# Performance work log

Measured on AMD Instinct MI355X. Metric: run time of the kernel, lower is better.

The kernel has to match this reference:

```python
import jax, jax.numpy as jnp
import numpy as np

NODE_NUM = 6
C_IN = 1024
B = 16384
N_OPS = 9
TAU = 10.0
EPS = 1e-5
ACTS = (jax.nn.relu, jax.nn.sigmoid, jnp.tanh)


def setup_inputs() -> dict:
    key = jax.random.key(0)
    k = jax.random.split(key, 12)
    n_edges = NODE_NUM * (NODE_NUM + 1) // 2  # 21
    nB = n_edges - NODE_NUM  # 15 edges with cin=cout=C_IN//2

    def w(kk, shape, fan_in):
        return jax.random.normal(kk, shape, jnp.float32) / np.float32(np.sqrt(fan_in))

    return {
        "x": jax.random.normal(k[0], (B, C_IN), jnp.float32),
        "arch_params": 0.001 * jax.random.normal(k[1], (n_edges, N_OPS), jnp.float32),
        "gumbel": jax.random.gumbel(k[2], (n_edges, N_OPS), jnp.float32),
        "dense_w_A": w(k[3], (NODE_NUM, 3, C_IN // 2, C_IN), C_IN),
        "dense_b_A": 0.01 * jax.random.normal(k[4], (NODE_NUM, 3, C_IN // 2), jnp.float32),
        "group_w_A": w(k[5], (NODE_NUM, 3, 4, C_IN // 8, C_IN // 4), C_IN // 4),
        "group_b_A": 0.01 * jax.random.normal(k[6], (NODE_NUM, 3, C_IN // 2), jnp.float32),
        "pool_w_A": w(k[7], (NODE_NUM, 2, C_IN // 2, C_IN), C_IN),
        "dense_w_B": w(k[8], (nB, 3, C_IN // 2, C_IN // 2), C_IN // 2),
        "dense_b_B": 0.01 * jax.random.normal(k[9], (nB, 3, C_IN // 2), jnp.float32),
        "group_w_B": w(k[10], (nB, 3, 4, C_IN // 8, C_IN // 8), C_IN // 8),
        "group_b_B": 0.01 * jax.random.normal(k[11], (nB, 3, C_IN // 2), jnp.float32),
    }


def _batchnorm(h):
    # training-mode BatchNorm2d on [B, C, 1, 1] == normalize over batch, affine-free
    m = jnp.mean(h, axis=0, keepdims=True)
    v = jnp.var(h, axis=0, keepdims=True)
    return (h - m) * jax.lax.rsqrt(v + EPS)


def _apply_edge(h, op_idx, wscale, dw, db, gw, gb, pw):
    # h: [B, cin]; dw: [3, cout, cin]; gw: [3, 4, cout//4, cin//4]; pw: [2, cout, cin] or None
    cout = dw.shape[1]

    def pool(p):
        def f(hh):
            # ReLU-Conv1x1-BN preprocess when cin != cout, else identity
            y = _batchnorm(jax.nn.relu(hh) @ pw[p].T) if pw is not None else hh
            if p == 0:  # avg_pool_3x3 on 1x1 spatial, pad=1, count_include_pad
                y = y / 9.0
            # p == 1: max_pool_3x3 on 1x1 spatial is identity
            return _batchnorm(y)  # MixedOp-appended BatchNorm2d(affine=False)
        return f

    def dense(a):
        return lambda hh: ACTS[a](hh @ dw[a].T + db[a])

    def gdense(a):
        def f(hh):
            hg = hh.reshape(hh.shape[0], 4, -1)  # [B, 4, cin//4]
            y = jnp.einsum('bgi,goi->bgo', hg, gw[a]).reshape(hh.shape[0], -1) + gb[a]
            return ACTS[a](y)
        return f

    zero = lambda hh: jnp.zeros((hh.shape[0], cout), hh.dtype)
    branches = [pool(0), pool(1), dense(0), dense(1), dense(2),
                gdense(0), gdense(1), gdense(2), zero]
    return jax.lax.switch(op_idx, branches, h) * wscale


def reference(x, arch_params, gumbel, dense_w_A, dense_b_A, group_w_A, group_b_A,
              pool_w_A, dense_w_B, dense_b_B, group_w_B, group_b_B):
    # GDAS gumbel-softmax hard routing (straight-through)
    logits = (jax.nn.log_softmax(arch_params, axis=1) + gumbel) / TAU
    prob = jax.nn.softmax(logits, axis=1)
    index = jnp.argmax(prob, axis=1)                      # [n_edges]
    one_h = jax.nn.one_hot(index, N_OPS, dtype=prob.dtype)
    hardwts = one_h - jax.lax.stop_gradient(prob) + prob  # [n_edges, N_OPS]

    # arch rows are indexed by sorted edge-key order, matching torch edge2index
    keys = sorted('{}->{}'.format(j, i + 1) for i in range(NODE_NUM) for j in range(i + 1))
    e2i = {kk: n for n, kk in enumerate(keys)}

    states = [x]
    a_ct = 0
    b_ct = 0
    for i in range(1, NODE_NUM + 1):
        acc = None
        for j in range(i):
            e = e2i['{}->{}'.format(j, i)]
            w_e = hardwts[e, index[e]]
            if j == 0:
                out = _apply_edge(states[0], index[e], w_e, dense_w_A[a_ct], dense_b_A[a_ct],
                                  group_w_A[a_ct], group_b_A[a_ct], pool_w_A[a_ct])
                a_ct += 1
            else:
                out = _apply_edge(states[j], index[e], w_e, dense_w_B[b_ct], dense_b_B[b_ct],
                                  group_w_B[b_ct], group_b_B[b_ct], None)
                b_ct += 1
            acc = out if acc is None else acc + out
        states.append(acc)
    return states[-1]  # [B, C_IN//2]; final_linear is never applied in forward()
```

## Files before the change

kernel.cpp:

```cpp
#include <hip/hip_runtime.h>

#define BATCH 16384
#define CH 512
#define EPSBN 1e-5f

typedef __attribute__((ext_vector_type(8))) short short8;
typedef __attribute__((ext_vector_type(4))) float f32x4;
typedef __attribute__((ext_vector_type(4))) unsigned short ushort4v;

#define GLOAD16(gp, lp) __builtin_amdgcn_global_load_lds( \
    (const __attribute__((address_space(1))) void*)(gp),  \
    (__attribute__((address_space(3))) void*)(lp), 16, 0, 0)

__constant__ int d_etab[6][6] = {
  {0,0,0,0,0,0},
  {1,6,0,0,0,0},
  {2,7,11,0,0,0},
  {3,8,12,15,0,0},
  {4,9,13,16,18,0},
  {5,10,14,17,19,20}};
__constant__ int d_bct[21] = {0,0,0,0,0,0, 0,1,3,6,10, 2,4,7,11, 5,8,12, 9,13, 14};

static __device__ __forceinline__ long woff(int e){
  return (e < 6) ? (long)e*524288 : 3145728L + (long)d_bct[e]*262144;
}

static __device__ __forceinline__ unsigned short f2b(float f){
  union { float f; unsigned u; } v; v.f = f;
  unsigned r = v.u + 0x7fffu + ((v.u >> 16) & 1u);
  return (unsigned short)(r >> 16);
}
static __device__ __forceinline__ float b2f(unsigned short u){
  union { unsigned u; float f; } v; v.u = ((unsigned)u) << 16; return v.f;
}
static __device__ __forceinline__ float actf(int act, float v){
  if (act == 0) return fmaxf(v, 0.f);
  if (act == 1) return 1.f/(1.f + __expf(-v));
  float e = __expf(2.f*v);
  return 1.f - 2.f/(e + 1.f);
}

__global__ void k_sentinel(float* out){ out[0] = 1.0e6f; }

__global__ void k_index(const float* __restrict__ ap, const float* __restrict__ gum,
                        int* __restrict__ idx, float* __restrict__ wsc){
  int e = threadIdx.x;
  if (e >= 21) return;
  const float* a = ap + e*9;
  const float* g = gum + e*9;
  float m = a[0];
  for (int o=1;o<9;o++) m = fmaxf(m, a[o]);
  float s = 0.f;
  for (int o=0;o<9;o++) s += expf(a[o]-m);
  float lse = m + logf(s);
  float lg[9]; float lm = -1e30f;
  for (int o=0;o<9;o++){ lg[o] = (a[o]-lse+g[o]) / 10.0f; lm = fmaxf(lm, lg[o]); }
  float ss = 0.f;
  for (int o=0;o<9;o++) ss += expf(lg[o]-lm);
  int bi = 0; float bp = -1.f;
  for (int o=0;o<9;o++){
    float p = expf(lg[o]-lm)/ss;
    if (p > bp){ bp = p; bi = o; }
  }
  idx[e] = bi;
  wsc[e] = (1.0f - bp) + bp;
}

__global__ void k_f2b4(const float* __restrict__ in, unsigned short* __restrict__ outp, long n4){
  long stride = (long)gridDim.x*blockDim.x;
  for (long i = (long)blockIdx.x*blockDim.x + threadIdx.x; i < n4; i += stride){
    const float4 v = ((const float4*)in)[i];
    ushort4v o;
    o[0] = f2b(v.x); o[1] = f2b(v.y); o[2] = f2b(v.z); o[3] = f2b(v.w);
    ((ushort4v*)outp)[i] = o;
  }
}

__global__ void k_wconv_all(const int* __restrict__ idxp,
                            const float* __restrict__ dwA, const float* __restrict__ pwA,
                            const float* __restrict__ gwA, const float* __restrict__ dwB,
                            const float* __restrict__ gwB,
                            unsigned short* __restrict__ Wball){
  int e = blockIdx.x >> 7;
  int blk = blockIdx.x & 127;
  int id = idxp[e];
  const float* src; long n;
  if (e < 6){
    int a = e;
    if (id >= 2 && id <= 4){ n = 524288; src = dwA + ((long)a*3 + (id-2))*n; }
    else if (id < 2)       { n = 524288; src = pwA + ((long)a*2 + id)*n; }
    else if (id <= 7)      { n = 131072; src = gwA + ((long)a*3 + (id-5))*131072; }
    else return;
  } else {
    int b = d_bct[e];
    if (id >= 2 && id <= 4)     { n = 262144; src = dwB + ((long)b*3 + (id-2))*n; }
    else if (id >= 5 && id <= 7){ n = 65536;  src = gwB + ((long)b*3 + (id-5))*65536; }
    else return;
  }
  unsigned short* dst = Wball + woff(e);
  long n4 = n >> 2;
  long stride = 128*256;
  for (long i = (long)blk*256 + threadIdx.x; i < n4; i += stride){
    const float4 v = ((const float4*)src)[i];
    ushort4v o;
    o[0] = f2b(v.x); o[1] = f2b(v.y); o[2] = f2b(v.z); o[3] = f2b(v.w);
    ((ushort4v*)dst)[i] = o;
  }
}

__global__ __launch_bounds__(512, 4) void k_gemm_pool(
    int node, const unsigned short* __restrict__ xb,
    const unsigned short* __restrict__ Wball, unsigned short* __restrict__ tmp,
    const int* __restrict__ idxp)
{
  int e = node - 1;
  int id = idxp[e];
  if (id >= 2) return;

  int bid = blockIdx.x;
  int lg = (bid & 7) * 64 + (bid >> 3);
  int rowTile = lg >> 2, colTile = lg & 3;
  int row0 = rowTile * 128, col0 = colTile * 128;

  int t = threadIdx.x;
  int lane = t & 63, wave = t >> 6;
  int wm = wave >> 2, wn = wave & 3;
  int l16 = lane & 15, lq = lane >> 4;

  __shared__ unsigned short LDS[24576];

  int ra = t >> 2;
  int ca = (((t & 3) ^ ((ra >> 1) & 3)) << 3);
  int aoff[4], boff[2];
  #pragma unroll
  for (int m=0;m<4;m++){ int R = wm*64 + m*16 + l16; aoff[m] = R*32 + ((lq ^ ((R>>1)&3))<<3); }
  #pragma unroll
  for (int n=0;n<2;n++){ int C = wn*32 + n*16 + l16; boff[n] = C*32 + ((lq ^ ((C>>1)&3))<<3); }

  const unsigned short* W = Wball + (long)e*524288 + (long)col0*1024;
  const unsigned short* gA = xb + (long)(row0 + ra)*1024 + ca;
  const unsigned short* gB = W  + (long)ra*1024 + ca;

  f32x4 acc[4][2];
  #pragma unroll
  for (int m=0;m<4;m++){ acc[m][0]=(f32x4){0,0,0,0}; acc[m][1]=(f32x4){0,0,0,0}; }

  auto STAGE = [&](int tile, int bsel){
    long kk = (long)tile*32;
    GLOAD16(gA + kk, &LDS[bsel*4096 + t*8]);
    GLOAD16(gB + kk, &LDS[12288 + bsel*4096 + t*8]);
  };

  const int nk = 32;
  STAGE(0, 0);
  STAGE(1, 1);
  int cb = 0;
  for (int kt = 0; kt < nk; ++kt){
    if (kt+1 < nk) { asm volatile("s_waitcnt vmcnt(2)" ::: "memory"); }
    else           { asm volatile("s_waitcnt vmcnt(0)" ::: "memory"); }
    __builtin_amdgcn_s_barrier();
    if (kt+2 < nk) STAGE(kt+2, (cb >= 1) ? cb-1 : cb+2);
    const unsigned short* pA = &LDS[cb*4096];
    const unsigned short* pB = &LDS[12288 + cb*4096];
    short8 a[4], b[2];
    #pragma unroll
    for (int m=0;m<4;m++){
      a[m] = *(const short8*)(pA + aoff[m]);
      #pragma unroll
      for (int q=0;q<8;q++) a[m][q] = (a[m][q] < (short)0) ? (short)0 : a[m][q];
    }
    #pragma unroll
    for (int n=0;n<2;n++) b[n] = *(const short8*)(pB + boff[n]);
    #pragma unroll
    for (int m=0;m<4;m++)
      #pragma unroll
      for (int n=0;n<2;n++)
        acc[m][n] = __builtin_amdgcn_mfma_f32_16x16x32_bf16(a[m], b[n], acc[m][n], 0,0,0);
    cb = (cb+1 == 3) ? 0 : cb+1;
  }

  #pragma unroll
  for (int n=0;n<2;n++){
    int cn = col0 + wn*32 + n*16 + l16;
    #pragma unroll
    for (int m=0;m<4;m++)
      #pragma unroll
      for (int r=0;r<4;r++){
        int row = row0 + wm*64 + m*16 + lq*4 + r;
        tmp[(long)row*CH + cn] = f2b(acc[m][n][r]);
      }
  }
}

__global__ __launch_bounds__(512) void k_stats_node(
    int node, const unsigned short* __restrict__ tmp,
    const unsigned short* __restrict__ sb0, const unsigned short* __restrict__ sb1,
    const unsigned short* __restrict__ sb2, const unsigned short* __restrict__ sb3,
    const unsigned short* __restrict__ sb4,
    float* __restrict__ part, const int* __restrict__ idxp)
{
  int c = threadIdx.x;
  for (int jj = 0; jj < node; ++jj){
    int e = d_etab[node-1][jj];
    if (idxp[e] >= 2) continue;
    const unsigned short* S;
    switch(jj){ case 0: S=tmp; break; case 1: S=sb0; break; case 2: S=sb1; break;
                case 3: S=sb2; break; case 4: S=sb3; break; default: S=sb4; }
    const unsigned short* p = S + (long)blockIdx.x*128*CH + c;
    float s = 0.f, q = 0.f;
    for (int r = 0; r < 128; r++){ float v = b2f(p[(long)r*CH]); s += v; q += v*v; }
    long o = (((long)jj*128 + blockIdx.x)*CH + c)*2;
    part[o] = s; part[o+1] = q;
  }
}

__global__ __launch_bounds__(512) void k_stats2_node(
    int node, const float* __restrict__ part,
    float* __restrict__ alphaAll, float* __restrict__ mvalAll,
    const int* __restrict__ idxp)
{
  int c = threadIdx.x;
  for (int jj = 0; jj < node; ++jj){
    int e = d_etab[node-1][jj];
    int id = idxp[e];
    if (id >= 2) continue;
    float s = 0.f, q = 0.f;
    for (int b = 0; b < 128; b++){
      long o = (((long)jj*128 + b)*CH + c)*2;
      s += part[o]; q += part[o+1];
    }
    float m = s * (1.f/16384.f);
    float v = q * (1.f/16384.f) - m*m;
    v = fmaxf(v, 0.f);
    float al;
    if (jj == 0){
      float s1 = rsqrtf(v + EPSBN);
      float vz = v / (v + EPSBN);
      al = (id==0) ? (s1 * (1.f/9.f) * rsqrtf(vz*(1.f/81.f) + EPSBN))
                   : (s1 * rsqrtf(vz + EPSBN));
    } else {
      al = (id==0) ? ((1.f/9.f) * rsqrtf(v*(1.f/81.f) + EPSBN))
                   : rsqrtf(v + EPSBN);
    }
    alphaAll[(long)e*CH + c] = al;
    mvalAll[(long)e*CH + c] = m;
  }
}

__global__ __launch_bounds__(512, 4) void k_fused(
    int node,
    const unsigned short* __restrict__ xb,
    const unsigned short* __restrict__ sb0, const unsigned short* __restrict__ sb1,
    const unsigned short* __restrict__ sb2, const unsigned short* __restrict__ sb3,
    const unsigned short* __restrict__ sb4,
    unsigned short* __restrict__ sbout, float* __restrict__ outf,
    const unsigned short* __restrict__ tmp, const unsigned short* __restrict__ Wball,
    const float* __restrict__ dbA, const float* __restrict__ gbA,
    const float* __restrict__ dbB, const float* __restrict__ gbB,
    const float* __restrict__ alphaAll, const float* __restrict__ mvalAll,
    const int* __restrict__ idxp, const float* __restrict__ wscp)
{
  int bid = blockIdx.x;
  int lg = (bid & 7) * 64 + (bid >> 3);
  int rowTile = lg >> 2, colTile = lg & 3;
  int row0 = rowTile * 128, col0 = colTile * 128;

  int t = threadIdx.x;
  int lane = t & 63, wave = t >> 6;
  int wm = wave >> 2, wn = wave & 3;
  int l16 = lane & 15, lq = lane >> 4;

  __shared__ unsigned short LDS[24576];

  int ra = t >> 2;
  int ca = (((t & 3) ^ ((ra >> 1) & 3)) << 3);
  int aoff[4], boff[2];
  #pragma unroll
  for (int m=0;m<4;m++){ int R = wm*64 + m*16 + l16; aoff[m] = R*32 + ((lq ^ ((R>>1)&3))<<3); }
  #pragma unroll
  for (int n=0;n<2;n++){ int C = wn*32 + n*16 + l16; boff[n] = C*32 + ((lq ^ ((C>>1)&3))<<3); }

  f32x4 facc[4][2];
  #pragma unroll
  for (int m=0;m<4;m++){ facc[m][0]=(f32x4){0,0,0,0}; facc[m][1]=(f32x4){0,0,0,0}; }

  for (int jj = 0; jj < node; ++jj){
    int e = d_etab[node-1][jj];
    int id = idxp[e];
    if (id == 8) continue;
    float we = wscp[e];

    const unsigned short* st;
    switch(jj){ case 0: st=xb; break; case 1: st=sb0; break; case 2: st=sb1; break;
                case 3: st=sb2; break; case 4: st=sb3; break; default: st=sb4; }

    if (id < 2){
      const unsigned short* S = (jj==0) ? tmp : st;
      const float* al = alphaAll + (long)e*CH;
      const float* mv = mvalAll + (long)e*CH;
      #pragma unroll
      for (int n=0;n<2;n++){
        int cn = col0 + wn*32 + n*16 + l16;
        float a_n = al[cn], m_n = mv[cn];
        #pragma unroll
        for (int m=0;m<4;m++){
          int rowb = row0 + wm*64 + m*16 + lq*4;
          #pragma unroll
          for (int r=0;r<4;r++)
            facc[m][n][r] += we * (b2f(S[(long)(rowb+r)*CH + cn]) - m_n) * a_n;
        }
      }
      continue;
    }

    bool grp = (id >= 5);
    int cin = (jj==0) ? 1024 : 512;
    int K = grp ? (cin >> 2) : cin;
    int act = grp ? id - 5 : id - 2;
    const unsigned short* Abase = st + (grp ? (long)colTile*K : 0);
    const unsigned short* Wbase = Wball + woff(e) + (long)col0*K;
    const float* bias;
    if (jj == 0) bias = (grp ? gbA : dbA) + ((long)e*3 + act)*CH;
    else         bias = (grp ? gbB : dbB) + ((long)d_bct[e]*3 + act)*CH;

    const unsigned short* gA = Abase + (long)(row0 + ra)*cin + ca;
    const unsigned short* gB = Wbase + (long)ra*K + ca;

    f32x4 acc[4][2];
    #pragma unroll
    for (int m=0;m<4;m++){ acc[m][0]=(f32x4){0,0,0,0}; acc[m][1]=(f32x4){0,0,0,0}; }

    auto STAGE = [&](int tile, int bsel){
      long kk = (long)tile*32;
      GLOAD16(gA + kk, &LDS[bsel*4096 + t*8]);
      GLOAD16(gB + kk, &LDS[12288 + bsel*4096 + t*8]);
    };

    int nk = K >> 5;
    __builtin_amdgcn_s_barrier();
    STAGE(0, 0);
    STAGE(1, 1);
    int cb = 0;
    for (int kt = 0; kt < nk; ++kt){
      if (kt+1 < nk) { asm volatile("s_waitcnt vmcnt(2)" ::: "memory"); }
      else           { asm volatile("s_waitcnt vmcnt(0)" ::: "memory"); }
      __builtin_amdgcn_s_barrier();
      if (kt+2 < nk) STAGE(kt+2, (cb >= 1) ? cb-1 : cb+2);
      const unsigned short* pA = &LDS[cb*4096];
      const unsigned short* pB = &LDS[12288 + cb*4096];
      short8 a[4], b[2];
      #pragma unroll
      for (int m=0;m<4;m++) a[m] = *(const short8*)(pA + aoff[m]);
      #pragma unroll
      for (int n=0;n<2;n++) b[n] = *(const short8*)(pB + boff[n]);
      #pragma unroll
      for (int m=0;m<4;m++)
        #pragma unroll
        for (int n=0;n<2;n++)
          acc[m][n] = __builtin_amdgcn_mfma_f32_16x16x32_bf16(a[m], b[n], acc[m][n], 0,0,0);
      cb = (cb+1 == 3) ? 0 : cb+1;
    }

    #pragma unroll
    for (int n=0;n<2;n++){
      int cn = col0 + wn*32 + n*16 + l16;
      float bv = bias[cn];
      #pragma unroll
      for (int m=0;m<4;m++)
        #pragma unroll
        for (int r=0;r<4;r++)
          facc[m][n][r] += we * actf(act, acc[m][n][r] + bv);
    }
  }

  #pragma unroll
  for (int n=0;n<2;n++){
    int cn = col0 + wn*32 + n*16 + l16;
    #pragma unroll
    for (int m=0;m<4;m++){
      int rowb = row0 + wm*64 + m*16 + lq*4;
      #pragma unroll
      for (int r=0;r<4;r++){
        long off = (long)(rowb+r)*CH + cn;
        if (node == 6) outf[off] = facc[m][n][r];
        else           sbout[off] = f2b(facc[m][n][r]);
      }
    }
  }
}

extern "C" void kernel_launch(void* const* d_in, const int* in_sizes, int n_in,
                              void* d_out, int out_size, void* d_ws, size_t ws_size,
                              hipStream_t stream)
{
  const float* x   = (const float*)d_in[0];
  const float* ap  = (const float*)d_in[1];
  const float* gum = (const float*)d_in[2];
  const float* dwA = (const float*)d_in[3];
  const float* dbA = (const float*)d_in[4];
  const float* gwA = (const float*)d_in[5];
  const float* gbA = (const float*)d_in[6];
  const float* pwA = (const float*)d_in[7];
  const float* dwB = (const float*)d_in[8];
  const float* dbB = (const float*)d_in[9];
  const float* gwB = (const float*)d_in[10];
  const float* gbB = (const float*)d_in[11];
  float* out = (float*)d_out;

  char* ws = (char*)d_ws;
  size_t cur = 0;
  auto alloc = [&](size_t bytes)->void*{
    size_t o = cur; cur += (bytes + 255) & ~(size_t)255; return (void*)(ws + o);
  };
  int*   idx      = (int*)  alloc(21*sizeof(int));
  float* wsc      = (float*)alloc(21*sizeof(float));
  float* alphaAll = (float*)alloc((size_t)21*CH*sizeof(float));
  float* mvalAll  = (float*)alloc((size_t)21*CH*sizeof(float));
  float* part     = (float*)alloc((size_t)6*128*CH*2*sizeof(float));
  unsigned short* Wball = (unsigned short*)alloc((size_t)7077888*sizeof(unsigned short));
  unsigned short* tmp   = (unsigned short*)alloc((size_t)BATCH*CH*sizeof(unsigned short));
  unsigned short* xb    = (unsigned short*)alloc((size_t)BATCH*1024*sizeof(unsigned short));
  unsigned short* sb[5];
  for (int i=0;i<5;i++)
    sb[i] = (unsigned short*)alloc((size_t)BATCH*CH*sizeof(unsigned short));

  if (cur > ws_size){
    hipLaunchKernelGGL(k_sentinel, dim3(1), dim3(1), 0, stream, out);
    return;
  }

  hipLaunchKernelGGL(k_f2b4, dim3(2048), dim3(256), 0, stream, x, xb, (long)BATCH*1024/4);
  hipLaunchKernelGGL(k_index, dim3(1), dim3(32), 0, stream, ap, gum, idx, wsc);
  hipLaunchKernelGGL(k_wconv_all, dim3(21*128), dim3(256), 0, stream,
                     idx, dwA, pwA, gwA, dwB, gwB, Wball);

  for (int node = 1; node <= 6; node++){
    hipLaunchKernelGGL(k_gemm_pool, dim3(512), dim3(512), 0, stream,
                       node, xb, Wball, tmp, idx);
    hipLaunchKernelGGL(k_stats_node, dim3(128), dim3(512), 0, stream,
                       node, tmp, sb[0], sb[1], sb[2], sb[3], sb[4], part, idx);
    hipLaunchKernelGGL(k_stats2_node, dim3(1), dim3(512), 0, stream,
                       node, part, alphaAll, mvalAll, idx);
    hipLaunchKernelGGL(k_fused, dim3(512), dim3(512), 0, stream,
                       node, xb, sb[0], sb[1], sb[2], sb[3], sb[4],
                       (node < 6) ? sb[node-1] : sb[0], out,
                       tmp, Wball, dbA, gbA, dbB, gbB,
                       alphaAll, mvalAll, idx, wsc);
  }
}
```

Measured before the change: 420.0 us.

## Load GEMM weight fragments directly to registers, stage only activations in LDS

In both the pool-preprocess GEMM and the fused node GEMM, the weight (B) operand is now read straight from global memory into registers, double-buffered across two k-steps. Only the activation (A) tile still goes through LDS via global_load_lds, which halves shared memory per block and removes the B-side LDS reads. The loop is unrolled by two and uses sched_barriers and vmcnt waits to overlap the register loads with MFMA work. The tradeoffs are uncoalesced 16-byte per-lane weight loads, more register pressure, and tighter vmcnt accounting that assumes a specific ordering of outstanding loads.

```diff
diff --git a/kernel.cpp b/kernel.cpp
--- a/kernel.cpp
+++ b/kernel.cpp
@@ -127,56 +127,69 @@
   int wm = wave >> 2, wn = wave & 3;
   int l16 = lane & 15, lq = lane >> 4;
 
-  __shared__ unsigned short LDS[24576];
+  __shared__ unsigned short LDS[12288];
 
   int ra = t >> 2;
   int ca = (((t & 3) ^ ((ra >> 1) & 3)) << 3);
-  int aoff[4], boff[2];
+  int aoff[4];
   #pragma unroll
   for (int m=0;m<4;m++){ int R = wm*64 + m*16 + l16; aoff[m] = R*32 + ((lq ^ ((R>>1)&3))<<3); }
-  #pragma unroll
-  for (int n=0;n<2;n++){ int C = wn*32 + n*16 + l16; boff[n] = C*32 + ((lq ^ ((C>>1)&3))<<3); }
-
-  const unsigned short* W = Wball + (long)e*524288 + (long)col0*1024;
-  const unsigned short* gA = xb + (long)(row0 + ra)*1024 + ca;
-  const unsigned short* gB = W  + (long)ra*1024 + ca;
+
+  const int K = 1024;
+  const unsigned short* Wbase = Wball + (long)e*524288 + (long)col0*K;
+  const unsigned short* bp0 = Wbase + (long)(wn*32 +  0 + l16)*K + lq*8;
+  const unsigned short* bp1 = Wbase + (long)(wn*32 + 16 + l16)*K + lq*8;
+  const unsigned short* gA = xb + (long)(row0 + ra)*K + ca;
 
   f32x4 acc[4][2];
   #pragma unroll
   for (int m=0;m<4;m++){ acc[m][0]=(f32x4){0,0,0,0}; acc[m][1]=(f32x4){0,0,0,0}; }
 
-  auto STAGE = [&](int tile, int bsel){
-    long kk = (long)tile*32;
-    GLOAD16(gA + kk, &LDS[bsel*4096 + t*8]);
-    GLOAD16(gB + kk, &LDS[12288 + bsel*4096 + t*8]);
+  auto COMPUTE = [&](const unsigned short* pA, const short8* b){
+    short8 a[4];
+    #pragma unroll
+    for (int m=0;m<4;m++){
+      a[m] = *(const short8*)(pA + aoff[m]);
+      #pragma unroll
+      for (int q=0;q<8;q++) a[m][q] = (a[m][q] < (short)0) ? (short)0 : a[m][q];
+    }
+    #pragma unroll
+    for (int m=0;m<4;m++)
+      #pragma unroll
+      for (int n=0;n<2;n++)
+        acc[m][n] = __builtin_amdgcn_mfma_f32_16x16x32_bf16(a[m], b[n], acc[m][n], 0,0,0);
   };
 
   const int nk = 32;
-  STAGE(0, 0);
-  STAGE(1, 1);
-  int cb = 0;
-  for (int kt = 0; kt < nk; ++kt){
-    if (kt+1 < nk) { asm volatile("s_waitcnt vmcnt(2)" ::: "memory"); }
+  short8 br0[2], br1[2];
+  br0[0] = *(const short8*)(bp0);
+  br0[1] = *(const short8*)(bp1);
+  __builtin_amdgcn_sched_barrier(0);
+  GLOAD16(gA,          &LDS[t*8]);
+  GLOAD16(gA + 32,     &LDS[4096 + t*8]);
+
+  int c0 = 0;
+  for (int kt = 0; kt < nk; kt += 2){
+    int c1 = c0+1; if (c1==3) c1=0;
+    int c2 = c1+1; if (c2==3) c2=0;
+    asm volatile("s_waitcnt vmcnt(1)" ::: "memory");
+    __builtin_amdgcn_s_barrier();
+    br1[0] = *(const short8*)(bp0 + (kt+1)*32);
+    br1[1] = *(const short8*)(bp1 + (kt+1)*32);
+    __builtin_amdgcn_sched_barrier(0);
+    if (kt+2 < nk) GLOAD16(gA + (long)(kt+2)*32, &LDS[c2*4096 + t*8]);
+    COMPUTE(&LDS[c0*4096], br0);
+    if (kt+2 < nk) { asm volatile("s_waitcnt vmcnt(1)" ::: "memory"); }
     else           { asm volatile("s_waitcnt vmcnt(0)" ::: "memory"); }
     __builtin_amdgcn_s_barrier();
-    if (kt+2 < nk) STAGE(kt+2, (cb >= 1) ? cb-1 : cb+2);
-    const unsigned short* pA = &LDS[cb*4096];
-    const unsigned short* pB = &LDS[12288 + cb*4096];
-    short8 a[4], b[2];
-    #pragma unroll
-    for (int m=0;m<4;m++){
-      a[m] = *(const short8*)(pA + aoff[m]);
-      #pragma unroll
-      for (int q=0;q<8;q++) a[m][q] = (a[m][q] < (short)0) ? (short)0 : a[m][q];
-    }
-    #pragma unroll
-    for (int n=0;n<2;n++) b[n] = *(const short8*)(pB + boff[n]);
-    #pragma unroll
-    for (int m=0;m<4;m++)
-      #pragma unroll
-      for (int n=0;n<2;n++)
-        acc[m][n] = __builtin_amdgcn_mfma_f32_16x16x32_bf16(a[m], b[n], acc[m][n], 0,0,0);
-    cb = (cb+1 == 3) ? 0 : cb+1;
+    if (kt+2 < nk){
+      br0[0] = *(const short8*)(bp0 + (kt+2)*32);
+      br0[1] = *(const short8*)(bp1 + (kt+2)*32);
+    }
+    __builtin_amdgcn_sched_barrier(0);
+    if (kt+3 < nk) GLOAD16(gA + (long)(kt+3)*32, &LDS[c0*4096 + t*8]);
+    COMPUTE(&LDS[c1*4096], br1);
+    c0 = c2;
   }
 
   #pragma unroll
@@ -270,15 +283,13 @@
   int wm = wave >> 2, wn = wave & 3;
   int l16 = lane & 15, lq = lane >> 4;
 
-  __shared__ unsigned short LDS[24576];
+  __shared__ unsigned short LDS[12288];
 
   int ra = t >> 2;
   int ca = (((t & 3) ^ ((ra >> 1) & 3)) << 3);
-  int aoff[4], boff[2];
+  int aoff[4];
   #pragma unroll
   for (int m=0;m<4;m++){ int R = wm*64 + m*16 + l16; aoff[m] = R*32 + ((lq ^ ((R>>1)&3))<<3); }
-  #pragma unroll
-  for (int n=0;n<2;n++){ int C = wn*32 + n*16 + l16; boff[n] = C*32 + ((lq ^ ((C>>1)&3))<<3); }
 
   f32x4 facc[4][2];
   #pragma unroll
@@ -323,42 +334,56 @@
     if (jj == 0) bias = (grp ? gbA : dbA) + ((long)e*3 + act)*CH;
     else         bias = (grp ? gbB : dbB) + ((long)d_bct[e]*3 + act)*CH;
 
+    const unsigned short* bp0 = Wbase + (long)(wn*32 +  0 + l16)*K + lq*8;
+    const unsigned short* bp1 = Wbase + (long)(wn*32 + 16 + l16)*K + lq*8;
     const unsigned short* gA = Abase + (long)(row0 + ra)*cin + ca;
-    const unsigned short* gB = Wbase + (long)ra*K + ca;
 
     f32x4 acc[4][2];
     #pragma unroll
     for (int m=0;m<4;m++){ acc[m][0]=(f32x4){0,0,0,0}; acc[m][1]=(f32x4){0,0,0,0}; }
 
-    auto STAGE = [&](int tile, int bsel){
-      long kk = (long)tile*32;
-      GLOAD16(gA + kk, &LDS[bsel*4096 + t*8]);
-      GLOAD16(gB + kk, &LDS[12288 + bsel*4096 + t*8]);
-    };
-
-    int nk = K >> 5;
-    __builtin_amdgcn_s_barrier();
-    STAGE(0, 0);
-    STAGE(1, 1);
-    int cb = 0;
-    for (int kt = 0; kt < nk; ++kt){
-      if (kt+1 < nk) { asm volatile("s_waitcnt vmcnt(2)" ::: "memory"); }
-      else           { asm volatile("s_waitcnt vmcnt(0)" ::: "memory"); }
-      __builtin_amdgcn_s_barrier();
-      if (kt+2 < nk) STAGE(kt+2, (cb >= 1) ? cb-1 : cb+2);
-      const unsigned short* pA = &LDS[cb*4096];
-      const unsigned short* pB = &LDS[12288 + cb*4096];
-      short8 a[4], b[2];
+    auto COMPUTE = [&](const unsigned short* pA, const short8* b){
+      short8 a[4];
       #pragma unroll
       for (int m=0;m<4;m++) a[m] = *(const short8*)(pA + aoff[m]);
-      #pragma unroll
-      for (int n=0;n<2;n++) b[n] = *(const short8*)(pB + boff[n]);
       #pragma unroll
       for (int m=0;m<4;m++)
         #pragma unroll
         for (int n=0;n<2;n++)
           acc[m][n] = __builtin_amdgcn_mfma_f32_16x16x32_bf16(a[m], b[n], acc[m][n], 0,0,0);
-      cb = (cb+1 == 3) ? 0 : cb+1;
+    };
+
+    int nk = K >> 5;
+    __builtin_amdgcn_s_barrier();
+    short8 br0[2], br1[2];
+    br0[0] = *(const short8*)(bp0);
+    br0[1] = *(const short8*)(bp1);
+    __builtin_amdgcn_sched_barrier(0);
+    GLOAD16(gA,      &LDS[t*8]);
+    GLOAD16(gA + 32, &LDS[4096 + t*8]);
+
+    int c0 = 0;
+    for (int kt = 0; kt < nk; kt += 2){
+      int c1 = c0+1; if (c1==3) c1=0;
+      int c2 = c1+1; if (c2==3) c2=0;
+      asm volatile("s_waitcnt vmcnt(1)" ::: "memory");
+      __builtin_amdgcn_s_barrier();
+      br1[0] = *(const short8*)(bp0 + (kt+1)*32);
+      br1[1] = *(const short8*)(bp1 + (kt+1)*32);
+      __builtin_amdgcn_sched_barrier(0);
+      if (kt+2 < nk) GLOAD16(gA + (long)(kt+2)*32, &LDS[c2*4096 + t*8]);
+      COMPUTE(&LDS[c0*4096], br0);
+      if (kt+2 < nk) { asm volatile("s_waitcnt vmcnt(1)" ::: "memory"); }
+      else           { asm volatile("s_waitcnt vmcnt(0)" ::: "memory"); }
+      __builtin_amdgcn_s_barrier();
+      if (kt+2 < nk){
+        br0[0] = *(const short8*)(bp0 + (kt+2)*32);
+        br0[1] = *(const short8*)(bp1 + (kt+2)*32);
+      }
+      __builtin_amdgcn_sched_barrier(0);
+      if (kt+3 < nk) GLOAD16(gA + (long)(kt+3)*32, &LDS[c0*4096 + t*8]);
+      COMPUTE(&LDS[c1*4096], br1);
+      c0 = c2;
     }
 
     #pragma unroll
```

Result: slower. 561.5 us (+33.7%).

## Batch all six x-input edge GEMMs into one launch before the node loop

Applied to the files above, without the earlier changes.

All six edges that read the input x (j=0) do not depend on earlier nodes, so one kernel now computes their GEMMs (pool, dense or grouped) together, writing pre-activation or activated results into per-node buffers. Their BN statistics are also gathered in one batched stats pass. The per-node fused kernel then only adds those precomputed outputs instead of redoing the K=1024 GEMM inside the sequential chain. This fills the GPU with a larger grid and removes per-node launches. In exchange it needs extra intermediate buffers and reuses the sb buffers in place, which makes the aliasing (pre and sbout pointing to the same buffer) subtle.

```diff
diff --git a/kernel.cpp b/kernel.cpp
--- a/kernel.cpp
+++ b/kernel.cpp
@@ -108,17 +108,28 @@
   }
 }
 
-__global__ __launch_bounds__(512, 4) void k_gemm_pool(
-    int node, const unsigned short* __restrict__ xb,
-    const unsigned short* __restrict__ Wball, unsigned short* __restrict__ tmp,
-    const int* __restrict__ idxp)
-{
-  int e = node - 1;
+__global__ __launch_bounds__(512, 4) void k_gemmA_all(
+    const unsigned short* __restrict__ xb, const unsigned short* __restrict__ Wball,
+    unsigned short* __restrict__ s0, unsigned short* __restrict__ s1,
+    unsigned short* __restrict__ s2, unsigned short* __restrict__ s3,
+    unsigned short* __restrict__ s4, unsigned short* __restrict__ pre6,
+    const float* __restrict__ dbA, const float* __restrict__ gbA,
+    const int* __restrict__ idxp, const float* __restrict__ wscp)
+{
+  int e = blockIdx.x >> 9;
   int id = idxp[e];
-  if (id >= 2) return;
-
-  int bid = blockIdx.x;
-  int lg = (bid & 7) * 64 + (bid >> 3);
+  if (id == 8) return;
+  unsigned short* target;
+  switch(e){ case 0: target=s0; break; case 1: target=s1; break; case 2: target=s2; break;
+             case 3: target=s3; break; case 4: target=s4; break; default: target=pre6; }
+  bool pool = (id < 2);
+  bool grp = (id >= 5);
+  int K = grp ? 256 : 1024;
+  int act = pool ? 0 : (grp ? id-5 : id-2);
+  float we = wscp[e];
+
+  int inner = blockIdx.x & 511;
+  int lg = (inner & 7) * 64 + (inner >> 3);
   int rowTile = lg >> 2, colTile = lg & 3;
   int row0 = rowTile * 128, col0 = colTile * 128;
 
@@ -137,9 +148,11 @@
   #pragma unroll
   for (int n=0;n<2;n++){ int C = wn*32 + n*16 + l16; boff[n] = C*32 + ((lq ^ ((C>>1)&3))<<3); }
 
-  const unsigned short* W = Wball + (long)e*524288 + (long)col0*1024;
-  const unsigned short* gA = xb + (long)(row0 + ra)*1024 + ca;
-  const unsigned short* gB = W  + (long)ra*1024 + ca;
+  const unsigned short* Abase = xb + (grp ? (long)colTile*K : 0);
+  const unsigned short* Wbase = Wball + (long)e*524288 + (long)col0*K;
+  const unsigned short* gA = Abase + (long)(row0 + ra)*1024 + ca;
+  const unsigned short* gB = Wbase + (long)ra*K + ca;
+  const float* bias = (grp ? gbA : dbA) + ((long)e*3 + act)*CH;
 
   f32x4 acc[4][2];
   #pragma unroll
@@ -151,7 +164,7 @@
     GLOAD16(gB + kk, &LDS[12288 + bsel*4096 + t*8]);
   };
 
-  const int nk = 32;
+  int nk = K >> 5;
   STAGE(0, 0);
   STAGE(1, 1);
   int cb = 0;
@@ -166,8 +179,10 @@
     #pragma unroll
     for (int m=0;m<4;m++){
       a[m] = *(const short8*)(pA + aoff[m]);
-      #pragma unroll
-      for (int q=0;q<8;q++) a[m][q] = (a[m][q] < (short)0) ? (short)0 : a[m][q];
+      if (pool){
+        #pragma unroll
+        for (int q=0;q<8;q++) a[m][q] = (a[m][q] < (short)0) ? (short)0 : a[m][q];
+      }
     }
     #pragma unroll
     for (int n=0;n<2;n++) b[n] = *(const short8*)(pB + boff[n]);
@@ -182,29 +197,77 @@
   #pragma unroll
   for (int n=0;n<2;n++){
     int cn = col0 + wn*32 + n*16 + l16;
+    float bv = pool ? 0.f : bias[cn];
     #pragma unroll
     for (int m=0;m<4;m++)
       #pragma unroll
       for (int r=0;r<4;r++){
         int row = row0 + wm*64 + m*16 + lq*4 + r;
-        tmp[(long)row*CH + cn] = f2b(acc[m][n][r]);
+        long off = (long)row*CH + cn;
+        if (pool) target[off] = f2b(acc[m][n][r]);
+        else      target[off] = f2b(we * actf(act, acc[m][n][r] + bv));
       }
   }
 }
 
-__global__ __launch_bounds__(512) void k_stats_node(
-    int node, const unsigned short* __restrict__ tmp,
+__global__ __launch_bounds__(512) void k_statsA(
+    const unsigned short* __restrict__ s0, const unsigned short* __restrict__ s1,
+    const unsigned short* __restrict__ s2, const unsigned short* __restrict__ s3,
+    const unsigned short* __restrict__ s4, const unsigned short* __restrict__ pre6,
+    float* __restrict__ part, const int* __restrict__ idxp)
+{
+  int e = blockIdx.x >> 7;
+  if (idxp[e] >= 2) return;
+  const unsigned short* S;
+  switch(e){ case 0: S=s0; break; case 1: S=s1; break; case 2: S=s2; break;
+             case 3: S=s3; break; case 4: S=s4; break; default: S=pre6; }
+  int blk = blockIdx.x & 127;
+  int c = threadIdx.x;
+  const unsigned short* p = S + (long)blk*128*CH + c;
+  float s = 0.f, q = 0.f;
+  for (int r = 0; r < 128; r++){ float v = b2f(p[(long)r*CH]); s += v; q += v*v; }
+  long o = (((long)e*128 + blk)*CH + c)*2;
+  part[o] = s; part[o+1] = q;
+}
+
+__global__ __launch_bounds__(512) void k_stats2A(
+    const float* __restrict__ part, float* __restrict__ alphaAll,
+    float* __restrict__ mvalAll, const int* __restrict__ idxp)
+{
+  int c = threadIdx.x;
+  for (int e = 0; e < 6; ++e){
+    int id = idxp[e];
+    if (id >= 2) continue;
+    float s = 0.f, q = 0.f;
+    for (int b = 0; b < 128; b++){
+      long o = (((long)e*128 + b)*CH + c)*2;
+      s += part[o]; q += part[o+1];
+    }
+    float m = s * (1.f/16384.f);
+    float v = q * (1.f/16384.f) - m*m;
+    v = fmaxf(v, 0.f);
+    float s1 = rsqrtf(v + EPSBN);
+    float vz = v / (v + EPSBN);
+    float al = (id==0) ? (s1 * (1.f/9.f) * rsqrtf(vz*(1.f/81.f) + EPSBN))
+                       : (s1 * rsqrtf(vz + EPSBN));
+    alphaAll[(long)e*CH + c] = al;
+    mvalAll[(long)e*CH + c] = m;
+  }
+}
+
+__global__ __launch_bounds__(512) void k_statsB_node(
+    int node,
     const unsigned short* __restrict__ sb0, const unsigned short* __restrict__ sb1,
     const unsigned short* __restrict__ sb2, const unsigned short* __restrict__ sb3,
     const unsigned short* __restrict__ sb4,
     float* __restrict__ part, const int* __restrict__ idxp)
 {
   int c = threadIdx.x;
-  for (int jj = 0; jj < node; ++jj){
+  for (int jj = 1; jj < node; ++jj){
     int e = d_etab[node-1][jj];
     if (idxp[e] >= 2) continue;
     const unsigned short* S;
-    switch(jj){ case 0: S=tmp; break; case 1: S=sb0; break; case 2: S=sb1; break;
+    switch(jj){ case 1: S=sb0; break; case 2: S=sb1; break;
                 case 3: S=sb2; break; case 4: S=sb3; break; default: S=sb4; }
     const unsigned short* p = S + (long)blockIdx.x*128*CH + c;
     float s = 0.f, q = 0.f;
@@ -214,13 +277,13 @@
   }
 }
 
-__global__ __launch_bounds__(512) void k_stats2_node(
+__global__ __launch_bounds__(512) void k_stats2B_node(
     int node, const float* __restrict__ part,
     float* __restrict__ alphaAll, float* __restrict__ mvalAll,
     const int* __restrict__ idxp)
 {
   int c = threadIdx.x;
-  for (int jj = 0; jj < node; ++jj){
+  for (int jj = 1; jj < node; ++jj){
     int e = d_etab[node-1][jj];
     int id = idxp[e];
     if (id >= 2) continue;
@@ -232,16 +295,8 @@
     float m = s * (1.f/16384.f);
     float v = q * (1.f/16384.f) - m*m;
     v = fmaxf(v, 0.f);
-    float al;
-    if (jj == 0){
-      float s1 = rsqrtf(v + EPSBN);
-      float vz = v / (v + EPSBN);
-      al = (id==0) ? (s1 * (1.f/9.f) * rsqrtf(vz*(1.f/81.f) + EPSBN))
-                   : (s1 * rsqrtf(vz + EPSBN));
-    } else {
-      al = (id==0) ? ((1.f/9.f) * rsqrtf(v*(1.f/81.f) + EPSBN))
-                   : rsqrtf(v + EPSBN);
-    }
+    float al = (id==0) ? ((1.f/9.f) * rsqrtf(v*(1.f/81.f) + EPSBN))
+                       : rsqrtf(v + EPSBN);
     alphaAll[(long)e*CH + c] = al;
     mvalAll[(long)e*CH + c] = m;
   }
@@ -249,13 +304,12 @@
 
 __global__ __launch_bounds__(512, 4) void k_fused(
     int node,
-    const unsigned short* __restrict__ xb,
+    const unsigned short* __restrict__ pre,
     const unsigned short* __restrict__ sb0, const unsigned short* __restrict__ sb1,
     const unsigned short* __restrict__ sb2, const unsigned short* __restrict__ sb3,
     const unsigned short* __restrict__ sb4,
     unsigned short* __restrict__ sbout, float* __restrict__ outf,
-    const unsigned short* __restrict__ tmp, const unsigned short* __restrict__ Wball,
-    const float* __restrict__ dbA, const float* __restrict__ gbA,
+    const unsigned short* __restrict__ Wball,
     const float* __restrict__ dbB, const float* __restrict__ gbB,
     const float* __restrict__ alphaAll, const float* __restrict__ mvalAll,
     const int* __restrict__ idxp, const float* __restrict__ wscp)
@@ -290,12 +344,43 @@
     if (id == 8) continue;
     float we = wscp[e];
 
+    if (jj == 0){
+      if (id < 2){
+        const float* al = alphaAll + (long)e*CH;
+        const float* mv = mvalAll + (long)e*CH;
+        #pragma unroll
+        for (int n=0;n<2;n++){
+          int cn = col0 + wn*32 + n*16 + l16;
+          float a_n = al[cn], m_n = mv[cn];
+          #pragma unroll
+          for (int m=0;m<4;m++){
+            int rowb = row0 + wm*64 + m*16 + lq*4;
+            #pragma unroll
+            for (int r=0;r<4;r++)
+              facc[m][n][r] += we * (b2f(pre[(long)(rowb+r)*CH + cn]) - m_n) * a_n;
+          }
+        }
+      } else {
+        #pragma unroll
+        for (int n=0;n<2;n++){
+          int cn = col0 + wn*32 + n*16 + l16;
+          #pragma unroll
+          for (int m=0;m<4;m++){
+            int rowb = row0 + wm*64 + m*16 + lq*4;
+            #pragma unroll
+            for (int r=0;r<4;r++)
+              facc[m][n][r] += b2f(pre[(long)(rowb+r)*CH + cn]);
+          }
+        }
+      }
+      continue;
+    }
+
     const unsigned short* st;
-    switch(jj){ case 0: st=xb; break; case 1: st=sb0; break; case 2: st=sb1; break;
+    switch(jj){ case 1: st=sb0; break; case 2: st=sb1; break;
                 case 3: st=sb2; break; case 4: st=sb3; break; default: st=sb4; }
 
     if (id < 2){
-      const unsigned short* S = (jj==0) ? tmp : st;
       const float* al = alphaAll + (long)e*CH;
       const float* mv = mvalAll + (long)e*CH;
       #pragma unroll
@@ -307,23 +392,20 @@
           int rowb = row0 + wm*64 + m*16 + lq*4;
           #pragma unroll
           for (int r=0;r<4;r++)
-            facc[m][n][r] += we * (b2f(S[(long)(rowb+r)*CH + cn]) - m_n) * a_n;
+            facc[m][n][r] += we * (b2f(st[(long)(rowb+r)*CH + cn]) - m_n) * a_n;
         }
       }
       continue;
     }
 
     bool grp = (id >= 5);
-    int cin = (jj==0) ? 1024 : 512;
-    int K = grp ? (cin >> 2) : cin;
+    int K = grp ? 128 : 512;
     int act = grp ? id - 5 : id - 2;
     const unsigned short* Abase = st + (grp ? (long)colTile*K : 0);
     const unsigned short* Wbase = Wball + woff(e) + (long)col0*K;
-    const float* bias;
-    if (jj == 0) bias = (grp ? gbA : dbA) + ((long)e*3 + act)*CH;
-    else         bias = (grp ? gbB : dbB) + ((long)d_bct[e]*3 + act)*CH;
-
-    const unsigned short* gA = Abase + (long)(row0 + ra)*cin + ca;
+    const float* bias = (grp ? gbB : dbB) + ((long)d_bct[e]*3 + act)*CH;
+
+    const unsigned short* gA = Abase + (long)(row0 + ra)*512 + ca;
     const unsigned short* gB = Wbase + (long)ra*K + ca;
 
     f32x4 acc[4][2];
@@ -418,7 +500,7 @@
   float* mvalAll  = (float*)alloc((size_t)21*CH*sizeof(float));
   float* part     = (float*)alloc((size_t)6*128*CH*2*sizeof(float));
   unsigned short* Wball = (unsigned short*)alloc((size_t)7077888*sizeof(unsigned short));
-  unsigned short* tmp   = (unsigned short*)alloc((size_t)BATCH*CH*sizeof(unsigned short));
+  unsigned short* pre6  = (unsigned short*)alloc((size_t)BATCH*CH*sizeof(unsigned short));
   unsigned short* xb    = (unsigned short*)alloc((size_t)BATCH*1024*sizeof(unsigned short));
   unsigned short* sb[5];
   for (int i=0;i<5;i++)
@@ -434,17 +516,26 @@
   hipLaunchKernelGGL(k_wconv_all, dim3(21*128), dim3(256), 0, stream,
                      idx, dwA, pwA, gwA, dwB, gwB, Wball);
 
-  for (int node = 1; node <= 6; node++){
-    hipLaunchKernelGGL(k_gemm_pool, dim3(512), dim3(512), 0, stream,
-                       node, xb, Wball, tmp, idx);
-    hipLaunchKernelGGL(k_stats_node, dim3(128), dim3(512), 0, stream,
-                       node, tmp, sb[0], sb[1], sb[2], sb[3], sb[4], part, idx);
-    hipLaunchKernelGGL(k_stats2_node, dim3(1), dim3(512), 0, stream,
+  hipLaunchKernelGGL(k_gemmA_all, dim3(6*512), dim3(512), 0, stream,
+                     xb, Wball, sb[0], sb[1], sb[2], sb[3], sb[4], pre6,
+                     dbA, gbA, idx, wsc);
+  hipLaunchKernelGGL(k_statsA, dim3(6*128), dim3(512), 0, stream,
+                     sb[0], sb[1], sb[2], sb[3], sb[4], pre6, part, idx);
+  hipLaunchKernelGGL(k_stats2A, dim3(1), dim3(512), 0, stream,
+                     part, alphaAll, mvalAll, idx);
+
+  hipLaunchKernelGGL(k_fused, dim3(512), dim3(512), 0, stream,
+                     1, sb[0], sb[0], sb[1], sb[2], sb[3], sb[4],
+                     sb[0], out, Wball, dbB, gbB, alphaAll, mvalAll, idx, wsc);
+  for (int node = 2; node <= 6; node++){
+    hipLaunchKernelGGL(k_statsB_node, dim3(128), dim3(512), 0, stream,
+                       node, sb[0], sb[1], sb[2], sb[3], sb[4], part, idx);
+    hipLaunchKernelGGL(k_stats2B_node, dim3(1), dim3(512), 0, stream,
                        node, part, alphaAll, mvalAll, idx);
+    const unsigned short* pre = (node < 6) ? sb[node-1] : pre6;
+    unsigned short* sbout = (node < 6) ? sb[node-1] : sb[0] ;
     hipLaunchKernelGGL(k_fused, dim3(512), dim3(512), 0, stream,
-                       node, xb, sb[0], sb[1], sb[2], sb[3], sb[4],
-                       (node < 6) ? sb[node-1] : sb[0], out,
-                       tmp, Wball, dbA, gbA, dbB, gbB,
-                       alphaAll, mvalAll, idx, wsc);
-  }
-}
+                       node, pre, sb[0], sb[1], sb[2], sb[3], sb[4],
+                       sbout, out, Wball, dbB, gbB, alphaAll, mvalAll, idx, wsc);
+  }
+}
```

New measurement: 455.2 us. 8.4% more time.
